# Kernel tuning notes

Hardware: AMD Instinct MI355X
Metric: run time of the kernel (lower is better)

## Reference

```python
import jax, jax.numpy as jnp
import numpy as np

WS = 14          # window size
NH = 12          # num heads
C = 768          # hidden dim
HD = C // NH     # head dim = 64
MLP = 3072       # mlp dim
EPS = 1e-6


def _layernorm(x, g, b):
    mu = jnp.mean(x, axis=-1, keepdims=True)
    var = jnp.mean(jnp.square(x - mu), axis=-1, keepdims=True)
    return (x - mu) * jax.lax.rsqrt(var + EPS) * g + b


def setup_inputs() -> dict:
    key = jax.random.key(0)
    ks = jax.random.split(key, 8)
    B, H, W = 8, 64, 64
    f32 = jnp.float32
    d = {}
    d["x"] = jax.random.normal(ks[0], (B, H, W, C), f32)
    d["ln1_g"] = jnp.ones((C,), f32)
    d["ln1_b"] = jnp.zeros((C,), f32)
    d["qkv_w"] = (jax.random.normal(ks[1], (C, 3 * C), f32) * 0.02)
    d["qkv_b"] = jnp.zeros((3 * C,), f32)
    d["proj_w"] = (jax.random.normal(ks[2], (C, C), f32) * 0.02)
    d["proj_b"] = jnp.zeros((C,), f32)
    d["rel_pos_h"] = (jax.random.normal(ks[3], (2 * WS - 1, HD), f32) * 0.02)
    d["rel_pos_w"] = (jax.random.normal(ks[4], (2 * WS - 1, HD), f32) * 0.02)
    d["ln2_g"] = jnp.ones((C,), f32)
    d["ln2_b"] = jnp.zeros((C,), f32)
    d["mlp_w1"] = (jax.random.normal(ks[5], (C, MLP), f32) * 0.02)
    d["mlp_b1"] = jnp.zeros((MLP,), f32)
    d["mlp_w2"] = (jax.random.normal(ks[6], (MLP, C), f32) * 0.02)
    d["mlp_b2"] = jnp.zeros((C,), f32)
    return d


def reference(x, ln1_g, ln1_b, qkv_w, qkv_b, proj_w, proj_b,
              rel_pos_h, rel_pos_w, ln2_g, ln2_b,
              mlp_w1, mlp_b1, mlp_w2, mlp_b2):
    B, H, W, _ = x.shape
    xn = _layernorm(x, ln1_g, ln1_b)

    # ---- window partition (pad to multiple of WS) ----
    pad_h = (-H) % WS
    pad_w = (-W) % WS
    Hp, Wp = H + pad_h, W + pad_w
    xp = jnp.pad(xn, ((0, 0), (0, pad_h), (0, pad_w), (0, 0)))
    # [B, Hp/WS, WS, Wp/WS, WS, C] -> [Bn, WS, WS, C]
    win = xp.reshape(B, Hp // WS, WS, Wp // WS, WS, C)
    win = win.transpose(0, 1, 3, 2, 4, 5).reshape(-1, WS, WS, C)
    Bn = win.shape[0]
    N = WS * WS

    # ---- attention with decomposed relative position bias ----
    qkv = win.reshape(Bn, N, C) @ qkv_w + qkv_b                 # [Bn, N, 3C]
    qkv = qkv.reshape(Bn, N, 3, NH, HD).transpose(2, 0, 3, 1, 4)
    qkv = qkv.reshape(3, Bn * NH, N, HD)
    q, k, v = qkv[0], qkv[1], qkv[2]

    scale = HD ** -0.5
    attn = jnp.einsum('bnd,bmd->bnm', q * scale, k)             # [Bn*NH, N, N]

    # rel coords: q_size == k_size == WS, rel_pos already has 2*WS-1 rows
    coords = jnp.arange(WS)[:, None] - jnp.arange(WS)[None, :] + (WS - 1)
    Rh = rel_pos_h[coords]                                      # [WS, WS, HD]
    Rw = rel_pos_w[coords]                                      # [WS, WS, HD]
    rq = q.reshape(Bn * NH, WS, WS, HD)
    rel_h = jnp.einsum('bhwc,hkc->bhwk', rq, Rh)                # [B', WS, WS, WS]
    rel_w = jnp.einsum('bhwc,wkc->bhwk', rq, Rw)
    attn = (attn.reshape(Bn * NH, WS, WS, WS, WS)
            + rel_h[:, :, :, :, None]
            + rel_w[:, :, :, None, :]).reshape(Bn * NH, N, N)

    attn = jax.nn.softmax(attn, axis=-1)
    out = jnp.einsum('bnm,bmd->bnd', attn, v)                   # [Bn*NH, N, HD]
    out = out.reshape(Bn, NH, WS, WS, HD).transpose(0, 2, 3, 1, 4).reshape(Bn, WS, WS, C)
    out = out @ proj_w + proj_b

    # ---- window unpartition ----
    out = out.reshape(B, Hp // WS, Wp // WS, WS, WS, C)
    out = out.transpose(0, 1, 3, 2, 4, 5).reshape(B, Hp, Wp, C)[:, :H, :W, :]

    x1 = x + out
    y = _layernorm(x1, ln2_g, ln2_b)
    y = jax.nn.gelu(y @ mlp_w1 + mlp_b1, approximate=False) @ mlp_w2 + mlp_b2
    return x1 + y
```

## Files before the change

kernel.cpp:

```cpp
#include <hip/hip_runtime.h>
#include <hip/hip_bf16.h>
#include <cstdint>
#include <cstddef>

using bf16 = __hip_bfloat16;
typedef __attribute__((ext_vector_type(8))) short short8;
typedef __attribute__((ext_vector_type(4))) float f32x4;

typedef __attribute__((address_space(1))) const void as1_void;
typedef __attribute__((address_space(3))) void as3_void;

__device__ __forceinline__ f32x4 mfma16x16x32(short8 a, short8 b, f32x4 c) {
  return __builtin_amdgcn_mfma_f32_16x16x32_bf16(a, b, c, 0, 0, 0);
}

__device__ __forceinline__ void gload_lds16(const void* g, void* l) {
  __builtin_amdgcn_global_load_lds((as1_void*)g, (as3_void*)l, 16, 0, 0);
}

__device__ __forceinline__ uint32_t cvtpk(float a, float b) {
  uint32_t r;
  asm("v_cvt_pk_bf16_f32 %0, %1, %2" : "=v"(r) : "v"(a), "v"(b));
  return r;
}

__device__ __forceinline__ float gelu_f(float v) {
  const float u = 0.7978845608f * v * (1.f + 0.044715f * v * v);
  const float e = __expf(-2.f * fabsf(u));
  const float t = (1.f - e) / (1.f + e);
  return 0.5f * v * (1.f + (u < 0.f ? -t : t));
}

static constexpr int MROWS = 39200;
static constexpr int MPAD  = 39296;
static constexpr int TOK2  = 32768;

__global__ __launch_bounds__(256)
void transpose_cast(const float* __restrict__ in, bf16* __restrict__ out, int K, int N) {
  __shared__ float t[32][33];
  const int tx = threadIdx.x & 31, ty = threadIdx.x >> 5;
  const int bx = blockIdx.x, by = blockIdx.y;
  const int x = bx * 32 + tx;
  for (int r = ty; r < 32; r += 8)
    t[r][tx] = in[(size_t)(by * 32 + r) * N + x];
  __syncthreads();
  const int xo = by * 32 + tx;
  for (int r = ty; r < 32; r += 8)
    out[(size_t)(bx * 32 + r) * K + xo] = __float2bfloat16(t[tx][r]);
}

__global__ __launch_bounds__(256)
void ln1_partition(const float* __restrict__ x, const float* __restrict__ g,
                   const float* __restrict__ bb, bf16* __restrict__ out) {
  const int token = blockIdx.x * 4 + (threadIdx.x >> 6);
  const int lane = threadIdx.x & 63;
  const int win = token / 196, tok = token % 196;
  const int b_ = win / 25, wh = (win / 5) % 5, ww = win % 5;
  const int i = tok / 14, j = tok % 14;
  const int h = wh * 14 + i, w = ww * 14 + j;
  bf16* o = out + (size_t)token * 768;
  if (h >= 64 || w >= 64) {
    for (int t = 0; t < 12; ++t) o[lane + 64 * t] = __float2bfloat16(0.f);
    return;
  }
  const float* src = x + ((size_t)((b_ * 64 + h) * 64 + w)) * 768;
  float vals[12], s = 0.f, ss = 0.f;
  #pragma unroll
  for (int t = 0; t < 12; ++t) {
    float v = src[lane + 64 * t];
    vals[t] = v; s += v; ss += v * v;
  }
  #pragma unroll
  for (int d = 32; d > 0; d >>= 1) { s += __shfl_xor(s, d); ss += __shfl_xor(ss, d); }
  const float mu = s * (1.f / 768.f);
  const float var = ss * (1.f / 768.f) - mu * mu;
  const float inv = rsqrtf(var + 1e-6f);
  #pragma unroll
  for (int t = 0; t < 12; ++t) {
    const int c = lane + 64 * t;
    o[c] = __float2bfloat16((vals[t] - mu) * inv * g[c] + bb[c]);
  }
}

__global__ __launch_bounds__(256)
void ln2_kernel(const float* __restrict__ x1, const float* __restrict__ g,
                const float* __restrict__ bb, bf16* __restrict__ out) {
  const int token = blockIdx.x * 4 + (threadIdx.x >> 6);
  const int lane = threadIdx.x & 63;
  const float* src = x1 + (size_t)token * 768;
  bf16* o = out + (size_t)token * 768;
  float vals[12], s = 0.f, ss = 0.f;
  #pragma unroll
  for (int t = 0; t < 12; ++t) {
    float v = src[lane + 64 * t];
    vals[t] = v; s += v; ss += v * v;
  }
  #pragma unroll
  for (int d = 32; d > 0; d >>= 1) { s += __shfl_xor(s, d); ss += __shfl_xor(ss, d); }
  const float mu = s * (1.f / 768.f);
  const float var = ss * (1.f / 768.f) - mu * mu;
  const float inv = rsqrtf(var + 1e-6f);
  #pragma unroll
  for (int t = 0; t < 12; ++t) {
    const int c = lane + 64 * t;
    o[c] = __float2bfloat16((vals[t] - mu) * inv * g[c] + bb[c]);
  }
}

template<int EPI>
__global__ __launch_bounds__(256)
void gemm_bf16(const bf16* __restrict__ A, const bf16* __restrict__ Bt,
               const float* __restrict__ bias, int K, int Mreal,
               const float* __restrict__ fin, float* __restrict__ fout,
               bf16* __restrict__ ob0, bf16* __restrict__ ob1, bf16* __restrict__ ob2) {
  __shared__ __align__(16) bf16 SMEM[16384];
  bf16* const lA0 = SMEM;
  bf16* const lA1 = SMEM + 4096;
  bf16* const lB0 = SMEM + 8192;
  bf16* const lB1 = SMEM + 12288;
  const int tid = threadIdx.x;
  const int lane = tid & 63, wv = tid >> 6;
  const int lr = lane & 15, hi = lane >> 4;
  const int wm = wv >> 1, wn = wv & 1;

  const int gx = gridDim.x;
  const int nwg = gx * gridDim.y;
  int lin = blockIdx.y * gx + blockIdx.x;
  {
    const int q8 = nwg >> 3, r8 = nwg & 7;
    const int xcd = lin & 7, pos = lin >> 3;
    lin = (xcd < r8 ? xcd * (q8 + 1) : r8 * (q8 + 1) + (xcd - r8) * q8) + pos;
  }
  const size_t arow0 = (size_t)(lin / gx) * 128;
  const size_t brow0 = (size_t)(lin % gx) * 128;
  f32x4 acc[4][4] = {};

  auto stage = [&](bf16* bufA, bf16* bufB, int kt) {
    const int k0 = kt * 32;
    #pragma unroll
    for (int it = 0; it < 2; ++it) {
      const int seg = it * 256 + tid;
      const int row = seg >> 2, kq = seg & 3;
      const size_t dst = (size_t)(it * 256 + wv * 64) * 8;
      if constexpr (EPI == 1) {
        const int k = k0 + kq * 8;
        gload_lds16(A + ((size_t)(k >> 6) * MPAD + arow0 + row) * 64 + (k & 63), bufA + dst);
      } else {
        gload_lds16(A + (arow0 + row) * K + k0 + kq * 8, bufA + dst);
      }
      gload_lds16(Bt + (brow0 + row) * K + k0 + kq * 8, bufB + dst);
    }
  };
  auto compute = [&](const bf16* bufA, const bf16* bufB) {
    short8 af[4], bfr[4];
    #pragma unroll
    for (int m = 0; m < 4; ++m) af[m] = *(const short8*)&bufA[(wm * 64 + m * 16 + lr) * 32 + hi * 8];
    #pragma unroll
    for (int n = 0; n < 4; ++n) bfr[n] = *(const short8*)&bufB[(wn * 64 + n * 16 + lr) * 32 + hi * 8];
    #pragma unroll
    for (int m = 0; m < 4; ++m)
      #pragma unroll
      for (int n = 0; n < 4; ++n)
        acc[m][n] = mfma16x16x32(af[m], bfr[n], acc[m][n]);
  };

  const int nt = K >> 5;
  stage(lA0, lB0, 0);
  __syncthreads();
  for (int t = 0; t < nt; t += 2) {
    if (t + 1 < nt) stage(lA1, lB1, t + 1);
    compute(lA0, lB0);
    __syncthreads();
    if (t + 2 < nt) stage(lA0, lB0, t + 2);
    compute(lA1, lB1);
    __syncthreads();
  }

  if constexpr (EPI == 0 || EPI == 2) {
    bf16* ct = SMEM;
    #pragma unroll
    for (int n = 0; n < 4; ++n) {
      const int col = wn * 64 + n * 16 + lr;
      const float bv = bias[(int)brow0 + col];
      #pragma unroll
      for (int m = 0; m < 4; ++m) {
        #pragma unroll
        for (int e = 0; e < 4; ++e) {
          const int row = wm * 64 + m * 16 + hi * 4 + e;
          float v = acc[m][n][e] + bv;
          if constexpr (EPI == 2) v = gelu_f(v);
          const int byte = (row << 8) + (col << 1);
          *(bf16*)((char*)ct + (byte ^ ((row & 7) << 5))) = __float2bfloat16(v);
        }
      }
    }
    __syncthreads();
    #pragma unroll
    for (int i = 0; i < 8; ++i) {
      const int lin16 = i * 256 + tid;
      const int row = lin16 >> 4;
      const int u   = lin16 & 15;
      const int byte = (row << 8) + (u << 4);
      const short8 val = *(const short8*)((char*)ct + (byte ^ ((row & 7) << 5)));
      const int grow = (int)arow0 + row;
      const int gcol = (int)brow0 + u * 8;
      if constexpr (EPI == 0) {
        if (grow < Mreal) {
          const int which = gcol / 768, head = (gcol >> 6) % 12, d = gcol & 63;
          bf16* dstb = (which == 0) ? ob0 : ((which == 1) ? ob1 : ob2);
          *(short8*)&dstb[((size_t)head * MPAD + grow) * 64 + d] = val;
        }
      } else {
        *(short8*)&ob0[(size_t)grow * 3072 + gcol] = val;
      }
    }
  } else {
    #pragma unroll
    for (int n = 0; n < 4; ++n) {
      const int col = (int)brow0 + wn * 64 + n * 16 + lr;
      const float bv = bias[col];
      #pragma unroll
      for (int m = 0; m < 4; ++m) {
        #pragma unroll
        for (int e = 0; e < 4; ++e) {
          const int row = (int)arow0 + wm * 64 + m * 16 + hi * 4 + e;
          const float v = acc[m][n][e] + bv;
          if constexpr (EPI == 1) {
            if (row < Mreal) {
              const int win = row / 196, tok = row % 196;
              const int b_ = win / 25, wh = (win / 5) % 5, ww = win % 5;
              const int i = tok / 14, j = tok % 14;
              const int h = wh * 14 + i, w = ww * 14 + j;
              if (h < 64 && w < 64) {
                const size_t idx = ((size_t)((b_ * 64 + h) * 64 + w)) * 768 + col;
                fout[idx] = fin[idx] + v;
              }
            }
          } else {
            const size_t idx = (size_t)row * 768 + col;
            fout[idx] = fin[idx] + v;
          }
        }
      }
    }
  }
}

__global__ __launch_bounds__(512, 2)
void attn_kernel(const bf16* __restrict__ qb, const bf16* __restrict__ kb,
                 const bf16* __restrict__ vb, const float* __restrict__ rph,
                 const float* __restrict__ rpw, bf16* __restrict__ aout) {
  __shared__ __align__(16) char SM[65248];
  bf16* pbh    = (bf16*)SM;
  bf16* pbw    = (bf16*)(SM + 4096);
  bf16* Gh     = (bf16*)(SM + 8192);
  bf16* Gw     = (bf16*)(SM + 23168);
  char* klds   = SM;
  char* vtb    = SM + 25600;
  bf16* relh_s = (bf16*)(SM + 54272);
  bf16* relw_s = (bf16*)(SM + 59760);

  const int bh = blockIdx.x;
  const int win = bh / 12, head = bh % 12;
  const size_t base = ((size_t)head * MPAD + win * 196) * 64;
  const bf16* Q  = qb + base;
  const bf16* Kp = kb + base;
  const bf16* Vp = vb + base;
  const int tid = threadIdx.x, lane = tid & 63, wv = tid >> 6;
  const int lr = lane & 15, hi = lane >> 4;

  for (int i = tid; i < 32 * 64; i += 512) {
    const int r = i >> 6, c = i & 63;
    const bool ok = r < 27;
    pbh[i] = __float2bfloat16(ok ? rph[r * 64 + c] : 0.f);
    pbw[i] = __float2bfloat16(ok ? rpw[r * 64 + c] : 0.f);
  }
  __syncthreads();
  {
    short8 bh00 = *(const short8*)&pbh[(lr) * 64 + hi * 8];
    short8 bh01 = *(const short8*)&pbh[(lr) * 64 + 32 + hi * 8];
    short8 bh10 = *(const short8*)&pbh[(16 + lr) * 64 + hi * 8];
    short8 bh11 = *(const short8*)&pbh[(16 + lr) * 64 + 32 + hi * 8];
    short8 bw00 = *(const short8*)&pbw[(lr) * 64 + hi * 8];
    short8 bw01 = *(const short8*)&pbw[(lr) * 64 + 32 + hi * 8];
    short8 bw10 = *(const short8*)&pbw[(16 + lr) * 64 + hi * 8];
    short8 bw11 = *(const short8*)&pbw[(16 + lr) * 64 + 32 + hi * 8];
    for (int mt = wv; mt < 13; mt += 8) {
      const short8 a0 = *(const short8*)&Q[(mt * 16 + lr) * 64 + hi * 8];
      const short8 a1 = *(const short8*)&Q[(mt * 16 + lr) * 64 + 32 + hi * 8];
      f32x4 g0 = {}, g1 = {}, g2 = {}, g3 = {};
      g0 = mfma16x16x32(a0, bh00, g0); g0 = mfma16x16x32(a1, bh01, g0);
      g1 = mfma16x16x32(a0, bh10, g1); g1 = mfma16x16x32(a1, bh11, g1);
      g2 = mfma16x16x32(a0, bw00, g2); g2 = mfma16x16x32(a1, bw01, g2);
      g3 = mfma16x16x32(a0, bw10, g3); g3 = mfma16x16x32(a1, bw11, g3);
      #pragma unroll
      for (int e = 0; e < 4; ++e) {
        const int row = mt * 16 + hi * 4 + e;
        Gh[row * 36 + lr]      = __float2bfloat16(g0[e]);
        Gh[row * 36 + 16 + lr] = __float2bfloat16(g1[e]);
        Gw[row * 36 + lr]      = __float2bfloat16(g2[e]);
        Gw[row * 36 + 16 + lr] = __float2bfloat16(g3[e]);
      }
    }
  }
  __syncthreads();
  bf16 ghr[6], gwr[6];
  #pragma unroll
  for (int t = 0; t < 6; ++t) {
    const int i = tid + t * 512;
    if (i < 196 * 14) {
      const int q = i / 14, kk = i - (i / 14) * 14;
      const int rh = q / 14 - kk + 13;
      const int rw2 = q - (q / 14) * 14 - kk + 13;
      ghr[t] = Gh[q * 36 + rh];
      gwr[t] = Gw[q * 36 + rw2];
    }
  }
  __syncthreads();
  #pragma unroll
  for (int t = 0; t < 6; ++t) {
    const int i = tid + t * 512;
    if (i < 196 * 14) { relh_s[i] = ghr[t]; relw_s[i] = gwr[t]; }
  }
  for (int c = wv; c < 25; c += 8) {
    const int row = c * 8 + (lane >> 3);
    const int ch  = (lane & 7) ^ (row & 7);
    gload_lds16(Kp + row * 64 + ch * 8, klds + c * 1024);
  }
  for (int i = tid; i < 196 * 8; i += 512) {
    const int key = i >> 3, dg = (i & 7) * 8;
    const short8 v = *(const short8*)&Vp[key * 64 + dg];
    #pragma unroll
    for (int j = 0; j < 8; ++j) {
      const int idx = (dg + j) * 448 + key * 2;
      *(bf16*)(vtb + (idx ^ (j << 4))) = ((const bf16*)&v)[j];
    }
  }
  for (int i = tid; i < 64 * 28; i += 512) {
    const int d = i / 28, key = 196 + i - (i / 28) * 28;
    const int idx = d * 448 + key * 2;
    *(bf16*)(vtb + (idx ^ ((d & 7) << 4))) = __float2bfloat16(0.f);
  }
  __syncthreads();

  for (int qt = wv; qt < 13; qt += 8) {
    const int q = qt * 16 + lr;
    const int qc = q < 196 ? q : 195;
    const short8 bq0 = *(const short8*)&Q[(qt * 16 + lr) * 64 + hi * 8];
    const short8 bq1 = *(const short8*)&Q[(qt * 16 + lr) * 64 + 32 + hi * 8];
    f32x4 s[13];
    __builtin_amdgcn_s_setprio(1);
    #pragma unroll
    for (int nt = 0; nt < 13; ++nt) {
      const int key = nt * 16 + lr;
      const char* kr = klds + key * 128;
      const short8 ka0 = *(const short8*)(kr + (((hi) ^ (key & 7)) << 4));
      const short8 ka1 = *(const short8*)(kr + (((hi + 4) ^ (key & 7)) << 4));
      f32x4 z = {};
      z = mfma16x16x32(ka0, bq0, z);
      z = mfma16x16x32(ka1, bq1, z);
      s[nt] = z;
    }
    __builtin_amdgcn_s_setprio(0);
    float mx = -3.0e38f;
    #pragma unroll
    for (int nt = 0; nt < 13; ++nt) {
      #pragma unroll
      for (int e = 0; e < 4; ++e) {
        const int key = nt * 16 + hi * 4 + e;
        const int kh = key / 14, kw = key - kh * 14;
        float v = s[nt][e] * 0.125f + __bfloat162float(relh_s[qc * 14 + kh])
                                    + __bfloat162float(relw_s[qc * 14 + kw]);
        v = (key < 196) ? v : -3.0e38f;
        s[nt][e] = v;
        mx = fmaxf(mx, v);
      }
    }
    mx = fmaxf(mx, __shfl_xor(mx, 16));
    mx = fmaxf(mx, __shfl_xor(mx, 32));
    float sm = 0.f;
    uint32_t pk0[14], pk1[14];
    #pragma unroll
    for (int nt = 0; nt < 13; ++nt) {
      const float p0 = __expf(s[nt][0] - mx);
      const float p1 = __expf(s[nt][1] - mx);
      const float p2 = __expf(s[nt][2] - mx);
      const float p3 = __expf(s[nt][3] - mx);
      sm += (p0 + p1) + (p2 + p3);
      pk0[nt] = cvtpk(p0, p1);
      pk1[nt] = cvtpk(p2, p3);
    }
    pk0[13] = 0u; pk1[13] = 0u;
    sm += __shfl_xor(sm, 16);
    sm += __shfl_xor(sm, 32);
    const float rinv = 1.f / sm;
    f32x4 o[4] = {};
    #pragma unroll
    for (int kk = 0; kk < 7; ++kk) {
      const uint32_t x0 = pk0[2 * kk],     x1 = pk1[2 * kk];
      const uint32_t y0 = pk0[2 * kk + 1], y1 = pk1[2 * kk + 1];
      const uint32_t s0 = (hi < 2) ? y0 : x0, s1 = (hi < 2) ? y1 : x1;
      const uint32_t t0 = __shfl_xor(s0, 32), t1 = __shfl_xor(s1, 32);
      const uint32_t o0 = (hi < 2) ? x0 : y0, o1 = (hi < 2) ? x1 : y1;
      const bool sendOwn = (hi == 1) || (hi == 2);
      const uint32_t u0 = sendOwn ? o0 : t0, u1 = sendOwn ? o1 : t1;
      const uint32_t r0 = __shfl_xor(u0, 16), r1 = __shfl_xor(u1, 16);
      union { uint32_t u[4]; short8 v; } pf;
      pf.u[0] = (hi == 0) ? x0 : ((hi == 2) ? t0 : r0);
      pf.u[1] = (hi == 0) ? x1 : ((hi == 2) ? t1 : r1);
      pf.u[2] = (hi == 3) ? y0 : ((hi == 1) ? t0 : r0);
      pf.u[3] = (hi == 3) ? y1 : ((hi == 1) ? t1 : r1);
      __builtin_amdgcn_s_setprio(1);
      #pragma unroll
      for (int n2 = 0; n2 < 4; ++n2) {
        const int d = n2 * 16 + lr;
        const int idx = d * 448 + (kk * 32 + hi * 8) * 2;
        const short8 va = *(const short8*)(vtb + (idx ^ ((lr & 7) << 4)));
        o[n2] = mfma16x16x32(va, pf.v, o[n2]);
      }
      __builtin_amdgcn_s_setprio(0);
    }
    if (q < 196) {
      bf16* orow = aout + ((size_t)head * MPAD + win * 196 + q) * 64;
      #pragma unroll
      for (int n2 = 0; n2 < 4; ++n2) {
        uint32_t d0 = cvtpk(o[n2][0] * rinv, o[n2][1] * rinv);
        uint32_t d1 = cvtpk(o[n2][2] * rinv, o[n2][3] * rinv);
        uint32_t* dst = (uint32_t*)&orow[n2 * 16 + hi * 4];
        dst[0] = d0; dst[1] = d1;
      }
    }
  }
}

extern "C" void kernel_launch(void* const* d_in, const int* in_sizes, int n_in,
                              void* d_out, int out_size, void* d_ws, size_t ws_size,
                              hipStream_t stream) {
  (void)in_sizes; (void)n_in; (void)out_size; (void)ws_size;
  const float* x      = (const float*)d_in[0];
  const float* ln1_g  = (const float*)d_in[1];
  const float* ln1_b  = (const float*)d_in[2];
  const float* qkv_w  = (const float*)d_in[3];
  const float* qkv_b  = (const float*)d_in[4];
  const float* proj_w = (const float*)d_in[5];
  const float* proj_b = (const float*)d_in[6];
  const float* rph    = (const float*)d_in[7];
  const float* rpw    = (const float*)d_in[8];
  const float* ln2_g  = (const float*)d_in[9];
  const float* ln2_b  = (const float*)d_in[10];
  const float* w1     = (const float*)d_in[11];
  const float* b1v    = (const float*)d_in[12];
  const float* w2     = (const float*)d_in[13];
  const float* b2v    = (const float*)d_in[14];
  float* outp = (float*)d_out;

  char* ws = (char*)d_ws;
  size_t off = 0;
  auto alloc = [&](size_t bytes) { char* p = ws + off; off += (bytes + 255) & ~(size_t)255; return p; };
  bf16* qkv_wt  = (bf16*)alloc((size_t)2304 * 768 * 2);
  bf16* proj_wt = (bf16*)alloc((size_t)768 * 768 * 2);
  bf16* w1t     = (bf16*)alloc((size_t)3072 * 768 * 2);
  bf16* w2t     = (bf16*)alloc((size_t)768 * 3072 * 2);
  const size_t szB1 = (size_t)MPAD * 768 * 2;
  const size_t szB2 = (size_t)TOK2 * 768 * 2;
  char* regB = alloc(szB1 > szB2 ? szB1 : szB2);
  const size_t szQKV = (size_t)3 * 12 * MPAD * 64 * 2;
  const size_t szH   = (size_t)TOK2 * 3072 * 2;
  char* regC = alloc(szQKV > szH ? szQKV : szH);

  bf16* xnwin   = (bf16*)regB;
  bf16* attnout = (bf16*)regB;
  bf16* xn2     = (bf16*)regB;
  bf16* qbuf    = (bf16*)regC;
  bf16* kbuf    = qbuf + (size_t)12 * MPAD * 64;
  bf16* vbuf    = kbuf + (size_t)12 * MPAD * 64;
  bf16* hbuf    = (bf16*)regC;

  transpose_cast<<<dim3(2304 / 32, 768 / 32), 256, 0, stream>>>(qkv_w, qkv_wt, 768, 2304);
  transpose_cast<<<dim3(768 / 32, 768 / 32), 256, 0, stream>>>(proj_w, proj_wt, 768, 768);
  transpose_cast<<<dim3(3072 / 32, 768 / 32), 256, 0, stream>>>(w1, w1t, 768, 3072);
  transpose_cast<<<dim3(768 / 32, 3072 / 32), 256, 0, stream>>>(w2, w2t, 3072, 768);

  ln1_partition<<<dim3(MROWS / 4), 256, 0, stream>>>(x, ln1_g, ln1_b, xnwin);

  gemm_bf16<0><<<dim3(2304 / 128, MPAD / 128), 256, 0, stream>>>(
      xnwin, qkv_wt, qkv_b, 768, MROWS, nullptr, nullptr, qbuf, kbuf, vbuf);

  attn_kernel<<<dim3(2400), 512, 0, stream>>>(qbuf, kbuf, vbuf, rph, rpw, attnout);

  gemm_bf16<1><<<dim3(768 / 128, MPAD / 128), 256, 0, stream>>>(
      attnout, proj_wt, proj_b, 768, MROWS, x, outp, nullptr, nullptr, nullptr);

  ln2_kernel<<<dim3(TOK2 / 4), 256, 0, stream>>>(outp, ln2_g, ln2_b, xn2);

  gemm_bf16<2><<<dim3(3072 / 128, TOK2 / 128), 256, 0, stream>>>(
      xn2, w1t, b1v, 768, TOK2, nullptr, nullptr, hbuf, nullptr, nullptr);
  gemm_bf16<3><<<dim3(768 / 128, TOK2 / 128), 256, 0, stream>>>(
      hbuf, w2t, b2v, 3072, TOK2, outp, outp, nullptr, nullptr, nullptr);
}
```

Baseline: 1.103 ms.

## Use 256x256-tile 8-wave GEMM with XCD remap for MLP layers

Adds a new gemm256 kernel with 256x256 output tiles, 512 threads, double-buffered direct-to-LDS loads with explicit waitcnt/barrier pipelining and s_setprio around MFMA bursts. Workgroup IDs are remapped so that neighbouring tiles land on the same XCD, which should improve L2 reuse. Both MLP GEMMs now use it, aiming for more operand reuse per LDS byte and less global traffic. The old kernel's EPI 2/3 paths are removed. The larger tile gives fewer workgroups (M=32768 → 128×12 and 128×3 tiles), which may hurt occupancy and tail balance, especially for the second GEMM.

After: 1.113 ms. About the same (+0.9%).

```diff
diff --git a/kernel.cpp b/kernel.cpp
--- a/kernel.cpp
+++ b/kernel.cpp
@@ -176,7 +176,7 @@
     __syncthreads();
   }
 
-  if constexpr (EPI == 0 || EPI == 2) {
+  if constexpr (EPI == 0) {
     bf16* ct = SMEM;
     #pragma unroll
     for (int n = 0; n < 4; ++n) {
@@ -187,8 +187,7 @@
         #pragma unroll
         for (int e = 0; e < 4; ++e) {
           const int row = wm * 64 + m * 16 + hi * 4 + e;
-          float v = acc[m][n][e] + bv;
-          if constexpr (EPI == 2) v = gelu_f(v);
+          const float v = acc[m][n][e] + bv;
           const int byte = (row << 8) + (col << 1);
           *(bf16*)((char*)ct + (byte ^ ((row & 7) << 5))) = __float2bfloat16(v);
         }
@@ -204,14 +203,10 @@
       const short8 val = *(const short8*)((char*)ct + (byte ^ ((row & 7) << 5)));
       const int grow = (int)arow0 + row;
       const int gcol = (int)brow0 + u * 8;
-      if constexpr (EPI == 0) {
-        if (grow < Mreal) {
-          const int which = gcol / 768, head = (gcol >> 6) % 12, d = gcol & 63;
-          bf16* dstb = (which == 0) ? ob0 : ((which == 1) ? ob1 : ob2);
-          *(short8*)&dstb[((size_t)head * MPAD + grow) * 64 + d] = val;
-        }
-      } else {
-        *(short8*)&ob0[(size_t)grow * 3072 + gcol] = val;
+      if (grow < Mreal) {
+        const int which = gcol / 768, head = (gcol >> 6) % 12, d = gcol & 63;
+        bf16* dstb = (which == 0) ? ob0 : ((which == 1) ? ob1 : ob2);
+        *(short8*)&dstb[((size_t)head * MPAD + grow) * 64 + d] = val;
       }
     }
   } else {
@@ -225,21 +220,143 @@
         for (int e = 0; e < 4; ++e) {
           const int row = (int)arow0 + wm * 64 + m * 16 + hi * 4 + e;
           const float v = acc[m][n][e] + bv;
-          if constexpr (EPI == 1) {
-            if (row < Mreal) {
-              const int win = row / 196, tok = row % 196;
-              const int b_ = win / 25, wh = (win / 5) % 5, ww = win % 5;
-              const int i = tok / 14, j = tok % 14;
-              const int h = wh * 14 + i, w = ww * 14 + j;
-              if (h < 64 && w < 64) {
-                const size_t idx = ((size_t)((b_ * 64 + h) * 64 + w)) * 768 + col;
-                fout[idx] = fin[idx] + v;
-              }
+          if (row < Mreal) {
+            const int win = row / 196, tok = row % 196;
+            const int b_ = win / 25, wh = (win / 5) % 5, ww = win % 5;
+            const int i = tok / 14, j = tok % 14;
+            const int h = wh * 14 + i, w = ww * 14 + j;
+            if (h < 64 && w < 64) {
+              const size_t idx = ((size_t)((b_ * 64 + h) * 64 + w)) * 768 + col;
+              fout[idx] = fin[idx] + v;
             }
-          } else {
-            const size_t idx = (size_t)row * 768 + col;
-            fout[idx] = fin[idx] + v;
           }
+        }
+      }
+    }
+  }
+}
+
+template<int EPI>
+__global__ __launch_bounds__(512)
+void gemm256(const bf16* __restrict__ A, const bf16* __restrict__ Bt,
+             const float* __restrict__ bias, int K,
+             const float* __restrict__ fin, float* __restrict__ fout,
+             bf16* __restrict__ ob0) {
+  __shared__ __align__(16) char SMEM[65536];
+  char* const bA0 = SMEM;
+  char* const bB0 = SMEM + 16384;
+  char* const bA1 = SMEM + 32768;
+  char* const bB1 = SMEM + 49152;
+  const int tid = threadIdx.x;
+  const int lane = tid & 63, wv = tid >> 6;
+  const int lr = lane & 15, hi = lane >> 4;
+  const int wm = wv >> 2, wn = wv & 3;
+
+  const int gx = gridDim.x;
+  const int nwg = gx * gridDim.y;
+  int lin = blockIdx.y * gx + blockIdx.x;
+  {
+    const int q8 = nwg >> 3, r8 = nwg & 7;
+    const int xcd = lin & 7, pos = lin >> 3;
+    lin = (xcd < r8 ? xcd * (q8 + 1) : r8 * (q8 + 1) + (xcd - r8) * q8) + pos;
+  }
+  const size_t arow0 = (size_t)(lin / gx) * 256;
+  const size_t brow0 = (size_t)(lin % gx) * 256;
+
+  f32x4 acc[8][4] = {};
+
+  auto stage = [&](int kt, char* dA, char* dB) {
+    const int k0 = kt * 32;
+    #pragma unroll
+    for (int j = 0; j < 2; ++j) {
+      const int unit = j * 512 + tid;
+      const int r = unit >> 2, s = unit & 3;
+      const int kk = ((s ^ (r & 3)) << 3);
+      gload_lds16(A + (arow0 + r) * (size_t)K + k0 + kk, dA + unit * 16);
+      gload_lds16(Bt + (brow0 + r) * (size_t)K + k0 + kk, dB + unit * 16);
+    }
+  };
+  auto compute = [&](const char* sA, const char* sB) {
+    short8 bfr[4];
+    #pragma unroll
+    for (int n = 0; n < 4; ++n) {
+      const int br = wn * 64 + n * 16 + lr;
+      bfr[n] = *(const short8*)(sB + br * 64 + ((hi ^ (br & 3)) << 4));
+    }
+    #pragma unroll
+    for (int m = 0; m < 8; ++m) {
+      const int ar = wm * 128 + m * 16 + lr;
+      const short8 af = *(const short8*)(sA + ar * 64 + ((hi ^ (ar & 3)) << 4));
+      #pragma unroll
+      for (int n = 0; n < 4; ++n)
+        acc[m][n] = mfma16x16x32(af, bfr[n], acc[m][n]);
+    }
+  };
+
+  const int nt = K >> 5;
+  stage(0, bA0, bB0);
+  stage(1, bA1, bB1);
+  for (int t = 0; t < nt; t += 2) {
+    asm volatile("s_waitcnt vmcnt(4)" ::: "memory");
+    __builtin_amdgcn_s_barrier();
+    __builtin_amdgcn_s_setprio(1);
+    compute(bA0, bB0);
+    __builtin_amdgcn_s_setprio(0);
+    asm volatile("s_waitcnt lgkmcnt(0)" ::: "memory");
+    __builtin_amdgcn_s_barrier();
+    if (t + 2 < nt) { stage(t + 2, bA0, bB0);
+                      asm volatile("s_waitcnt vmcnt(4)" ::: "memory"); }
+    else            { asm volatile("s_waitcnt vmcnt(0)" ::: "memory"); }
+    __builtin_amdgcn_s_barrier();
+    __builtin_amdgcn_s_setprio(1);
+    compute(bA1, bB1);
+    __builtin_amdgcn_s_setprio(0);
+    asm volatile("s_waitcnt lgkmcnt(0)" ::: "memory");
+    __builtin_amdgcn_s_barrier();
+    if (t + 3 < nt) stage(t + 3, bA1, bB1);
+  }
+
+  if constexpr (EPI == 2) {
+    char* ep = SMEM + wv * 8192;
+    #pragma unroll
+    for (int h = 0; h < 2; ++h) {
+      #pragma unroll
+      for (int m2 = 0; m2 < 4; ++m2) {
+        #pragma unroll
+        for (int n = 0; n < 4; ++n) {
+          const int col = n * 16 + lr;
+          const float bv = bias[(int)brow0 + wn * 64 + col];
+          #pragma unroll
+          for (int e = 0; e < 4; ++e) {
+            const int row_l = m2 * 16 + hi * 4 + e;
+            const float v = gelu_f(acc[h * 4 + m2][n][e] + bv);
+            *(bf16*)(ep + row_l * 128 + (((col >> 3) ^ (row_l & 7)) << 4) + ((col & 7) << 1))
+                = __float2bfloat16(v);
+          }
+        }
+      }
+      #pragma unroll
+      for (int p = 0; p < 8; ++p) {
+        const int row_l = p * 8 + (lane >> 3);
+        const int slot  = lane & 7;
+        const short8 val = *(const short8*)(ep + row_l * 128 + ((slot ^ (row_l & 7)) << 4));
+        const size_t grow = arow0 + wm * 128 + h * 64 + row_l;
+        const int gcol = (int)brow0 + wn * 64 + slot * 8;
+        *(short8*)&ob0[grow * 3072 + gcol] = val;
+      }
+    }
+  } else {
+    #pragma unroll
+    for (int n = 0; n < 4; ++n) {
+      const int col = (int)brow0 + wn * 64 + n * 16 + lr;
+      const float bv = bias[col];
+      #pragma unroll
+      for (int m = 0; m < 8; ++m) {
+        #pragma unroll
+        for (int e = 0; e < 4; ++e) {
+          const size_t row = arow0 + wm * 128 + m * 16 + hi * 4 + e;
+          const size_t idx = row * 768 + col;
+          fout[idx] = fin[idx] + acc[m][n][e] + bv;
         }
       }
     }
@@ -493,8 +610,8 @@
 
   ln2_kernel<<<dim3(TOK2 / 4), 256, 0, stream>>>(outp, ln2_g, ln2_b, xn2);
 
-  gemm_bf16<2><<<dim3(3072 / 128, TOK2 / 128), 256, 0, stream>>>(
-      xn2, w1t, b1v, 768, TOK2, nullptr, nullptr, hbuf, nullptr, nullptr);
-  gemm_bf16<3><<<dim3(768 / 128, TOK2 / 128), 256, 0, stream>>>(
-      hbuf, w2t, b2v, 3072, TOK2, outp, outp, nullptr, nullptr, nullptr);
-}
+  gemm256<2><<<dim3(3072 / 256, TOK2 / 256), 512, 0, stream>>>(
+      xn2, w1t, b1v, 768, nullptr, nullptr, hbuf);
+  gemm256<3><<<dim3(768 / 256, TOK2 / 256), 512, 0, stream>>>(
+      hbuf, w2t, b2v, 3072, outp, outp, nullptr);
+}
```
